# Performance work log

Measured on AMD Instinct MI355X. Metric: run time of the kernel, lower is better.

Reference implementation:

```python
import jax, jax.numpy as jnp
import numpy as np

EMBED = 2048
HEADS = 32
HEAD_DIM = EMBED // HEADS
ALPHA = 12.0
MAX_SEQ = 1024
GAMMA = -ALPHA / MAX_SEQ  # clipped softmax lower stretch
ETA = 1.0


def setup_inputs() -> dict:
    key = jax.random.key(0)
    ks = jax.random.split(key, 12)
    B, T, E, H, D = 4, 1024, EMBED, HEADS, HEAD_DIM
    s = 1.0 / np.sqrt(E)
    hidden_states = jax.random.normal(ks[0], (B, T, E), dtype=jnp.float32)
    # causal attention mask: True = attend
    causal = jnp.tril(jnp.ones((T, T), dtype=bool))
    attention_mask = jnp.broadcast_to(causal[None, None], (B, 1, T, T))
    Wq = jax.random.normal(ks[1], (E, E), dtype=jnp.float32) * s
    bq = jnp.zeros((E,), dtype=jnp.float32)
    Wk = jax.random.normal(ks[2], (E, E), dtype=jnp.float32) * s
    bk = jnp.zeros((E,), dtype=jnp.float32)
    Wv = jax.random.normal(ks[3], (E, E), dtype=jnp.float32) * s
    bv = jnp.zeros((E,), dtype=jnp.float32)
    Wo = jax.random.normal(ks[4], (E, E), dtype=jnp.float32) * s
    bo = jnp.zeros((E,), dtype=jnp.float32)
    gate_w = jax.random.normal(ks[5], (H, D), dtype=jnp.float32) * (1.0 / np.sqrt(D))
    gate_b = jnp.zeros((H,), dtype=jnp.float32)
    return {"hidden_states": hidden_states, "attention_mask": attention_mask,
            "Wq": Wq, "bq": bq, "Wk": Wk, "bk": bk, "Wv": Wv, "bv": bv,
            "Wo": Wo, "bo": bo, "gate_w": gate_w, "gate_b": gate_b}


def clipped_softmax(x, gamma, eta):
    p = jax.nn.softmax(x, axis=-1)
    return jnp.clip((eta - gamma) * p + gamma, 0.0, 1.0)


def reference(hidden_states, attention_mask, Wq, bq, Wk, bk, Wv, bv, Wo, bo, gate_w, gate_b):
    B, T, E = hidden_states.shape
    H, D = HEADS, HEAD_DIM
    scaling = D ** -0.5
    neg_min = jnp.finfo(hidden_states.dtype).min

    q = ((hidden_states @ Wq.T + bq) * scaling).reshape(B, T, H, D)
    k = (hidden_states @ Wk.T + bk).reshape(B, T, H, D)
    v = (hidden_states @ Wv.T + bv).reshape(B, T, H, D)

    # scores: [B,H,T,S]
    scores = jnp.einsum('bthd,bshd->bhts', q, k)
    mask_add = jnp.where(attention_mask, 0.0, neg_min)  # [B,1,T,S]
    scores = jnp.maximum(scores + mask_add, neg_min)

    probs = clipped_softmax(scores, GAMMA, ETA)

    attn_out = jnp.einsum('bhts,bshd->bhtd', probs, v)  # [B,H,T,D]

    # conditional_per_token gate: per-head Linear(head_dim -> 1), sigmoid
    x_heads = hidden_states.reshape(B, T, H, D)
    gate = jax.nn.sigmoid(jnp.einsum('bthd,hd->bht', x_heads, gate_w) + gate_b[None, :, None])
    attn_out = attn_out * gate[..., None]  # gate_scaling_factor = 1.0

    out = attn_out.transpose(0, 2, 1, 3).reshape(B, T, E)
    return out @ Wo.T + bo
```

## Files before the change

kernel.cpp:

```cpp
#include <hip/hip_runtime.h>
#include <hip/hip_bf16.h>

typedef unsigned short ushort_t;
using short8 = __attribute__((ext_vector_type(8))) short;
using f32x4  = __attribute__((ext_vector_type(4))) float;

constexpr int B_ = 4;
constexpr int T_ = 1024;
constexpr int E_ = 2048;
constexpr int H_ = 32;
constexpr int D_ = 64;
constexpr float GAMMA_  = -12.0f / 1024.0f;
constexpr float ONE_MG_ = 1.0f - GAMMA_;

__device__ __forceinline__ ushort_t f2bf(float f) {
  union { float f; unsigned int i; } x; x.f = f;
  unsigned int u = x.i;
  u += 0x7fffu + ((u >> 16) & 1u);
  return (ushort_t)(u >> 16);
}

__global__ __launch_bounds__(256) void f2bf_multi(
    const float* __restrict__ x,
    const float* __restrict__ Wq, const float* __restrict__ Wk,
    const float* __restrict__ Wv, const float* __restrict__ Wo,
    ushort_t* __restrict__ xb,
    ushort_t* __restrict__ wqb, ushort_t* __restrict__ wkb,
    ushort_t* __restrict__ wvb, ushort_t* __restrict__ wob) {
  const int i = blockIdx.x * 256 + threadIdx.x;
  const float* src; ushort_t* dst; int off;
  if (i < 2097152)      { src = x;  dst = xb;  off = i; }
  else if (i < 3145728) { src = Wq; dst = wqb; off = i - 2097152; }
  else if (i < 4194304) { src = Wk; dst = wkb; off = i - 3145728; }
  else if (i < 5242880) { src = Wv; dst = wvb; off = i - 4194304; }
  else                  { src = Wo; dst = wob; off = i - 5242880; }
  const float4 f = ((const float4*)src)[off];
  ushort4 u; u.x = f2bf(f.x); u.y = f2bf(f.y); u.z = f2bf(f.z); u.w = f2bf(f.w);
  ((ushort4*)dst)[off] = u;
}

__device__ __forceinline__ void gl_lds16(const ushort_t* g, ushort_t* l) {
  __builtin_amdgcn_global_load_lds(
      (const __attribute__((address_space(1))) void*)g,
      (__attribute__((address_space(3))) void*)l, 16, 0, 0);
}

__global__ __launch_bounds__(256) void gemm_qkv(
    const ushort_t* __restrict__ xb,
    const ushort_t* __restrict__ wq, const ushort_t* __restrict__ wk,
    const ushort_t* __restrict__ wv,
    const float* __restrict__ bq, const float* __restrict__ bk,
    const float* __restrict__ bv,
    ushort_t* __restrict__ qout, ushort_t* __restrict__ kout,
    ushort_t* __restrict__ vtout) {
  constexpr int K = 2048;
  __shared__ ushort_t As[128 * 32];
  __shared__ ushort_t Bs[128 * 32];
  const int which = blockIdx.x >> 4;
  const int colt  = blockIdx.x & 15;
  const ushort_t* Wt  = (which == 0) ? wq : (which == 1) ? wk : wv;
  const float*   bias = (which == 0) ? bq : (which == 1) ? bk : bv;
  const float    scale = (which == 0) ? 0.125f : 1.0f;

  const int tid = threadIdx.x;
  const int wave = tid >> 6, lane = tid & 63;
  const int lane15 = lane & 15, quad = lane >> 4;
  const int row0 = blockIdx.y * 128, col0 = colt * 128;
  const int srow = lane >> 2;
  const int scol = (lane & 3) * 8;
  const ushort_t* Ag0 = xb + (size_t)(row0 + wave * 32 + srow) * K + scol;
  const ushort_t* Ag1 = Ag0 + 16 * (size_t)K;
  const ushort_t* Bg0 = Wt + (size_t)(col0 + wave * 32 + srow) * K + scol;
  const ushort_t* Bg1 = Bg0 + 16 * (size_t)K;
  ushort_t* Al0 = &As[(wave * 32     ) * 32];
  ushort_t* Al1 = &As[(wave * 32 + 16) * 32];
  ushort_t* Bl0 = &Bs[(wave * 32     ) * 32];
  ushort_t* Bl1 = &Bs[(wave * 32 + 16) * 32];
  const int wr = wave >> 1, wc = wave & 1;
  const int q8 = quad * 8;

  f32x4 acc[4][4];
#pragma unroll
  for (int i = 0; i < 4; i++)
#pragma unroll
    for (int j = 0; j < 4; j++) acc[i][j] = (f32x4){0.f, 0.f, 0.f, 0.f};

  for (int k0 = 0; k0 < K; k0 += 32) {
    __syncthreads();
    gl_lds16(Ag0 + k0, Al0);
    gl_lds16(Ag1 + k0, Al1);
    gl_lds16(Bg0 + k0, Bl0);
    gl_lds16(Bg1 + k0, Bl1);
    __syncthreads();
    short8 a_f[4], b_f[4];
#pragma unroll
    for (int i = 0; i < 4; i++)
      a_f[i] = *(const short8*)&As[(wr * 64 + i * 16 + lane15) * 32 + q8];
#pragma unroll
    for (int j = 0; j < 4; j++)
      b_f[j] = *(const short8*)&Bs[(wc * 64 + j * 16 + lane15) * 32 + q8];
#pragma unroll
    for (int i = 0; i < 4; i++)
#pragma unroll
      for (int j = 0; j < 4; j++)
        acc[i][j] = __builtin_amdgcn_mfma_f32_16x16x32_bf16(
            a_f[i], b_f[j], acc[i][j], 0, 0, 0);
  }

  ushort_t* outp = (which == 0) ? qout : (which == 1) ? kout : vtout;
#pragma unroll
  for (int j = 0; j < 4; j++) {
    const int c = col0 + wc * 64 + j * 16 + lane15;
    const float bia = bias[c];
#pragma unroll
    for (int i = 0; i < 4; i++) {
#pragma unroll
      for (int reg = 0; reg < 4; reg++) {
        const int r = row0 + wr * 64 + i * 16 + quad * 4 + reg;
        const float val = (acc[i][j][reg] + bia) * scale;
        const int b = r >> 10, t = r & 1023, h = c >> 6, d = c & 63;
        if (which < 2)
          outp[(((size_t)(b * 32 + h)) * 1024 + t) * 64 + d] = f2bf(val);
        else
          outp[(((size_t)(b * 32 + h)) * 64 + d) * 1024 + t] = f2bf(val);
      }
    }
  }
}

__global__ __launch_bounds__(256) void gemm_out(
    const ushort_t* __restrict__ A, const ushort_t* __restrict__ Wt,
    const float* __restrict__ bias, float* __restrict__ Cout) {
  constexpr int K = 2048;
  __shared__ ushort_t As[128 * 32];
  __shared__ ushort_t Bs[128 * 32];
  const int tid = threadIdx.x;
  const int wave = tid >> 6, lane = tid & 63;
  const int lane15 = lane & 15, quad = lane >> 4;
  const int row0 = blockIdx.y * 128, col0 = blockIdx.x * 128;
  const int srow = lane >> 2;
  const int scol = (lane & 3) * 8;
  const ushort_t* Ag0 = A  + (size_t)(row0 + wave * 32 + srow) * K + scol;
  const ushort_t* Ag1 = Ag0 + 16 * (size_t)K;
  const ushort_t* Bg0 = Wt + (size_t)(col0 + wave * 32 + srow) * K + scol;
  const ushort_t* Bg1 = Bg0 + 16 * (size_t)K;
  ushort_t* Al0 = &As[(wave * 32     ) * 32];
  ushort_t* Al1 = &As[(wave * 32 + 16) * 32];
  ushort_t* Bl0 = &Bs[(wave * 32     ) * 32];
  ushort_t* Bl1 = &Bs[(wave * 32 + 16) * 32];
  const int wr = wave >> 1, wc = wave & 1;
  const int q8 = quad * 8;

  f32x4 acc[4][4];
#pragma unroll
  for (int i = 0; i < 4; i++)
#pragma unroll
    for (int j = 0; j < 4; j++) acc[i][j] = (f32x4){0.f, 0.f, 0.f, 0.f};

  for (int k0 = 0; k0 < K; k0 += 32) {
    __syncthreads();
    gl_lds16(Ag0 + k0, Al0);
    gl_lds16(Ag1 + k0, Al1);
    gl_lds16(Bg0 + k0, Bl0);
    gl_lds16(Bg1 + k0, Bl1);
    __syncthreads();
    short8 a_f[4], b_f[4];
#pragma unroll
    for (int i = 0; i < 4; i++)
      a_f[i] = *(const short8*)&As[(wr * 64 + i * 16 + lane15) * 32 + q8];
#pragma unroll
    for (int j = 0; j < 4; j++)
      b_f[j] = *(const short8*)&Bs[(wc * 64 + j * 16 + lane15) * 32 + q8];
#pragma unroll
    for (int i = 0; i < 4; i++)
#pragma unroll
      for (int j = 0; j < 4; j++)
        acc[i][j] = __builtin_amdgcn_mfma_f32_16x16x32_bf16(
            a_f[i], b_f[j], acc[i][j], 0, 0, 0);
  }

#pragma unroll
  for (int j = 0; j < 4; j++) {
    const int c = col0 + wc * 64 + j * 16 + lane15;
    const float bia = bias[c];
#pragma unroll
    for (int i = 0; i < 4; i++) {
#pragma unroll
      for (int reg = 0; reg < 4; reg++) {
        const int r = row0 + wr * 64 + i * 16 + quad * 4 + reg;
        Cout[(size_t)r * 2048 + c] = acc[i][j][reg] + bia;
      }
    }
  }
}

__global__ __launch_bounds__(256) void gates_kernel(
    const float* __restrict__ x, const float* __restrict__ gw,
    const float* __restrict__ gb, float* __restrict__ gates) {
  const int idx = blockIdx.x * 256 + threadIdx.x;
  const int h = idx & 31;
  const int bt = idx >> 5;
  const float* xp = x + (size_t)bt * E_ + h * D_;
  const float* wp = gw + h * D_;
  float s = 0.f;
#pragma unroll
  for (int d = 0; d < D_; d += 4) {
    const float4 xv = *(const float4*)&xp[d];
    const float4 wv = *(const float4*)&wp[d];
    s = fmaf(xv.x, wv.x, s); s = fmaf(xv.y, wv.y, s);
    s = fmaf(xv.z, wv.z, s); s = fmaf(xv.w, wv.w, s);
  }
  s += gb[h];
  gates[idx] = 1.0f / (1.0f + __expf(-s));
}

__global__ __launch_bounds__(256) void attn_mfma(
    const ushort_t* __restrict__ q, const ushort_t* __restrict__ k,
    const ushort_t* __restrict__ vt, const float* __restrict__ gates,
    ushort_t* __restrict__ attn_out) {
  __shared__ ushort_t Kt[64 * 72];
  __shared__ ushort_t Vt[64 * 72];
  __shared__ ushort_t Pb[4][16 * 72];

  const int tid = threadIdx.x;
  const int wave = tid >> 6, lane = tid & 63;
  const int l15 = lane & 15, quad = lane >> 4;
  const int bx = blockIdx.x;
  const int qt = 7 - (bx >> 7);
  const int bh = bx & 127;
  const int h = bh & 31, b = bh >> 5;
  const int t0 = qt * 128;
  const int qt8 = qt * 8;
  const ushort_t* qbase = q  + (size_t)bh * (T_ * D_);
  const ushort_t* kbase = k  + (size_t)bh * (T_ * D_);
  const ushort_t* vbase = vt + (size_t)bh * (D_ * T_);

  short8 qf[2][2];
#pragma unroll
  for (int s = 0; s < 2; s++) {
    const ushort_t* qp =
        qbase + (size_t)(t0 + s * 64 + wave * 16 + l15) * 64 + quad * 8;
    qf[s][0] = *(const short8*)qp;
    qf[s][1] = *(const short8*)(qp + 32);
  }

  const int srow = tid >> 2;
  const int scol = (tid & 3) * 16;
  const int nkt = 2 * qt + 2;

  float l_part[2][4] = {};

  for (int kt = 0; kt < nkt; kt++) {
    __syncthreads();
    {
      const ushort_t* kg = &kbase[(size_t)(kt * 64 + srow) * 64 + scol];
      ushort_t* kl = &Kt[srow * 72 + scol];
      *(short8*)kl = *(const short8*)kg;
      *(short8*)(kl + 8) = *(const short8*)(kg + 8);
    }
    __syncthreads();
#pragma unroll
    for (int s = 0; s < 2; s++) {
      const int rb = qt8 + s * 4 + wave;
      if (kt * 4 > rb) continue;
      f32x4 sc[4];
#pragma unroll
      for (int j = 0; j < 4; j++) {
        const int cb = kt * 4 + j;
        if (cb > rb) {
          sc[j] = (f32x4){-3.0e38f, -3.0e38f, -3.0e38f, -3.0e38f};
          continue;
        }
        const ushort_t* kp = &Kt[(j * 16 + l15) * 72 + quad * 8];
        const short8 kf0 = *(const short8*)kp;
        const short8 kf1 = *(const short8*)(kp + 32);
        f32x4 z = (f32x4){0.f, 0.f, 0.f, 0.f};
        z = __builtin_amdgcn_mfma_f32_16x16x32_bf16(qf[s][0], kf0, z, 0, 0, 0);
        z = __builtin_amdgcn_mfma_f32_16x16x32_bf16(qf[s][1], kf1, z, 0, 0, 0);
        if (cb == rb) {
#pragma unroll
          for (int r = 0; r < 4; r++)
            if (l15 > quad * 4 + r) z[r] = -3.0e38f;
        }
        sc[j] = z;
      }
#pragma unroll
      for (int r = 0; r < 4; r++)
        l_part[s][r] += __expf(sc[0][r]) + __expf(sc[1][r]) +
                        __expf(sc[2][r]) + __expf(sc[3][r]);
    }
  }

  float c1[2][4];
#pragma unroll
  for (int s = 0; s < 2; s++)
#pragma unroll
    for (int r = 0; r < 4; r++) {
      float e = l_part[s][r];
      e += __shfl_xor(e, 1); e += __shfl_xor(e, 2);
      e += __shfl_xor(e, 4); e += __shfl_xor(e, 8);
      c1[s][r] = ONE_MG_ / e;
    }

  f32x4 acc[2][4];
#pragma unroll
  for (int s = 0; s < 2; s++)
#pragma unroll
    for (int jd = 0; jd < 4; jd++) acc[s][jd] = (f32x4){0.f, 0.f, 0.f, 0.f};

  for (int kt = 0; kt < nkt; kt++) {
    __syncthreads();
    {
      const ushort_t* kg = &kbase[(size_t)(kt * 64 + srow) * 64 + scol];
      ushort_t* kl = &Kt[srow * 72 + scol];
      *(short8*)kl = *(const short8*)kg;
      *(short8*)(kl + 8) = *(const short8*)(kg + 8);
      const ushort_t* vg = &vbase[(size_t)srow * 1024 + kt * 64 + scol];
      ushort_t* vl = &Vt[srow * 72 + scol];
      *(short8*)vl = *(const short8*)vg;
      *(short8*)(vl + 8) = *(const short8*)(vg + 8);
    }
    __syncthreads();
#pragma unroll
    for (int s = 0; s < 2; s++) {
      const int rb = qt8 + s * 4 + wave;
      if (kt * 4 > rb) continue;
      f32x4 sc[4];
#pragma unroll
      for (int j = 0; j < 4; j++) {
        const int cb = kt * 4 + j;
        if (cb > rb) {
          sc[j] = (f32x4){-3.0e38f, -3.0e38f, -3.0e38f, -3.0e38f};
          continue;
        }
        const ushort_t* kp = &Kt[(j * 16 + l15) * 72 + quad * 8];
        const short8 kf0 = *(const short8*)kp;
        const short8 kf1 = *(const short8*)(kp + 32);
        f32x4 z = (f32x4){0.f, 0.f, 0.f, 0.f};
        z = __builtin_amdgcn_mfma_f32_16x16x32_bf16(qf[s][0], kf0, z, 0, 0, 0);
        z = __builtin_amdgcn_mfma_f32_16x16x32_bf16(qf[s][1], kf1, z, 0, 0, 0);
        if (cb == rb) {
#pragma unroll
          for (int r = 0; r < 4; r++)
            if (l15 > quad * 4 + r) z[r] = -3.0e38f;
        }
        sc[j] = z;
      }
      ushort_t* pb = &Pb[wave][0];
#pragma unroll
      for (int j = 0; j < 4; j++) {
#pragma unroll
        for (int r = 0; r < 4; r++) {
          float p = fmaf(c1[s][r], __expf(sc[j][r]), GAMMA_);
          p = fminf(fmaxf(p, 0.f), 1.f);
          pb[(quad * 4 + r) * 72 + j * 16 + l15] = f2bf(p);
        }
      }
      const short8 pf0 = *(const short8*)&pb[l15 * 72 + quad * 8];
      const short8 pf1 = *(const short8*)&pb[l15 * 72 + 32 + quad * 8];
#pragma unroll
      for (int jd = 0; jd < 4; jd++) {
        const ushort_t* vp = &Vt[(jd * 16 + l15) * 72 + quad * 8];
        const short8 vf0 = *(const short8*)vp;
        const short8 vf1 = *(const short8*)(vp + 32);
        acc[s][jd] =
            __builtin_amdgcn_mfma_f32_16x16x32_bf16(pf0, vf0, acc[s][jd], 0, 0, 0);
        acc[s][jd] =
            __builtin_amdgcn_mfma_f32_16x16x32_bf16(pf1, vf1, acc[s][jd], 0, 0, 0);
      }
    }
  }

#pragma unroll
  for (int s = 0; s < 2; s++) {
#pragma unroll
    for (int r = 0; r < 4; r++) {
      const int t = t0 + s * 64 + wave * 16 + quad * 4 + r;
      const float g = gates[((size_t)b * T_ + t) * H_ + h];
      ushort_t* op = attn_out + ((size_t)b * T_ + t) * E_ + h * 64;
#pragma unroll
      for (int jd = 0; jd < 4; jd++)
        op[jd * 16 + l15] = f2bf(acc[s][jd][r] * g);
    }
  }
}

extern "C" void kernel_launch(void* const* d_in, const int* in_sizes, int n_in,
                              void* d_out, int out_size, void* d_ws, size_t ws_size,
                              hipStream_t stream) {
  (void)in_sizes; (void)n_in; (void)out_size; (void)ws_size;
  const float* x  = (const float*)d_in[0];
  const float* Wq = (const float*)d_in[2];
  const float* bq = (const float*)d_in[3];
  const float* Wk = (const float*)d_in[4];
  const float* bk = (const float*)d_in[5];
  const float* Wv = (const float*)d_in[6];
  const float* bv = (const float*)d_in[7];
  const float* Wo = (const float*)d_in[8];
  const float* bo = (const float*)d_in[9];
  const float* gw = (const float*)d_in[10];
  const float* gb = (const float*)d_in[11];
  float* out = (float*)d_out;

  char* W = (char*)d_ws;
  ushort_t* xb  = (ushort_t*)(W + 0);
  ushort_t* wqb = (ushort_t*)(W + 16777216);
  ushort_t* wkb = (ushort_t*)(W + 25165824);
  ushort_t* wvb = (ushort_t*)(W + 33554432);
  ushort_t* wob = (ushort_t*)(W + 41943040);
  ushort_t* qb  = (ushort_t*)(W + 50331648);
  ushort_t* kb  = (ushort_t*)(W + 67108864);
  ushort_t* vtb = (ushort_t*)(W + 83886080);
  ushort_t* ab  = (ushort_t*)(W + 100663296);
  float*    gts = (float*)(W + 117440512);

  f2bf_multi<<<24576, 256, 0, stream>>>(x, Wq, Wk, Wv, Wo,
                                        xb, wqb, wkb, wvb, wob);

  gemm_qkv<<<dim3(48, 32), 256, 0, stream>>>(xb, wqb, wkb, wvb,
                                             bq, bk, bv, qb, kb, vtb);
  gates_kernel<<<512, 256, 0, stream>>>(x, gw, gb, gts);
  attn_mfma<<<1024, 256, 0, stream>>>(qb, kb, vtb, gts, ab);
  gemm_out<<<dim3(16, 32), 256, 0, stream>>>(ab, wob, bo, out);
}
```

Baseline: 426.6 us.

## Fold log2e into Q scale, sync-free first pass, truncating bf16 probs

Multiplies the Q projection scale by log2(e) so the softmax can use exp2f in place of __expf. The first denominator pass now reads K fragments straight from global memory with no LDS staging or barriers, and reuses each K fragment for both query sub-tiles. Probabilities are cast to bf16 by truncation instead of round-to-nearest, which is cheaper but adds a small downward bias. The risks are more global/L2 traffic in the first pass and a slight loss of accuracy.

```diff
diff --git a/kernel.cpp b/kernel.cpp
--- a/kernel.cpp
+++ b/kernel.cpp
@@ -12,12 +12,17 @@
 constexpr int D_ = 64;
 constexpr float GAMMA_  = -12.0f / 1024.0f;
 constexpr float ONE_MG_ = 1.0f - GAMMA_;
+constexpr float LOG2E_  = 1.44269504088896f;
 
 __device__ __forceinline__ ushort_t f2bf(float f) {
   union { float f; unsigned int i; } x; x.f = f;
   unsigned int u = x.i;
   u += 0x7fffu + ((u >> 16) & 1u);
   return (ushort_t)(u >> 16);
+}
+__device__ __forceinline__ ushort_t f2bf_trunc(float f) {
+  union { float f; unsigned int i; } x; x.f = f;
+  return (ushort_t)(x.i >> 16);
 }
 
 __global__ __launch_bounds__(256) void f2bf_multi(
@@ -60,7 +65,7 @@
   const int colt  = blockIdx.x & 15;
   const ushort_t* Wt  = (which == 0) ? wq : (which == 1) ? wk : wv;
   const float*   bias = (which == 0) ? bq : (which == 1) ? bk : bv;
-  const float    scale = (which == 0) ? 0.125f : 1.0f;
+  const float    scale = (which == 0) ? 0.125f * LOG2E_ : 1.0f;
 
   const int tid = threadIdx.x;
   const int wave = tid >> 6, lane = tid & 63;
@@ -247,8 +252,53 @@
   const int srow = tid >> 2;
   const int scol = (tid & 3) * 16;
   const int nkt = 2 * qt + 2;
+  const int rb1 = qt8 + 4 + wave;
 
   float l_part[2][4] = {};
+
+  for (int kt = 0; kt < nkt; kt++) {
+#pragma unroll
+    for (int j = 0; j < 4; j++) {
+      const int cb = kt * 4 + j;
+      if (cb > rb1) continue;
+      const ushort_t* kp =
+          kbase + (size_t)(kt * 64 + j * 16 + l15) * 64 + quad * 8;
+      const short8 kf0 = *(const short8*)kp;
+      const short8 kf1 = *(const short8*)(kp + 32);
+#pragma unroll
+      for (int s = 0; s < 2; s++) {
+        const int rb = qt8 + s * 4 + wave;
+        if (cb > rb) continue;
+        f32x4 z = (f32x4){0.f, 0.f, 0.f, 0.f};
+        z = __builtin_amdgcn_mfma_f32_16x16x32_bf16(qf[s][0], kf0, z, 0, 0, 0);
+        z = __builtin_amdgcn_mfma_f32_16x16x32_bf16(qf[s][1], kf1, z, 0, 0, 0);
+        if (cb == rb) {
+#pragma unroll
+          for (int r = 0; r < 4; r++)
+            if (l15 > quad * 4 + r) z[r] = -3.0e38f;
+        }
+#pragma unroll
+        for (int r = 0; r < 4; r++) l_part[s][r] += exp2f(z[r]);
+      }
+    }
+  }
+
+  float c1[2][4];
+#pragma unroll
+  for (int s = 0; s < 2; s++)
+#pragma unroll
+    for (int r = 0; r < 4; r++) {
+      float e = l_part[s][r];
+      e += __shfl_xor(e, 1); e += __shfl_xor(e, 2);
+      e += __shfl_xor(e, 4); e += __shfl_xor(e, 8);
+      c1[s][r] = ONE_MG_ / e;
+    }
+
+  f32x4 acc[2][4];
+#pragma unroll
+  for (int s = 0; s < 2; s++)
+#pragma unroll
+    for (int jd = 0; jd < 4; jd++) acc[s][jd] = (f32x4){0.f, 0.f, 0.f, 0.f};
 
   for (int kt = 0; kt < nkt; kt++) {
     __syncthreads();
@@ -257,6 +307,10 @@
       ushort_t* kl = &Kt[srow * 72 + scol];
       *(short8*)kl = *(const short8*)kg;
       *(short8*)(kl + 8) = *(const short8*)(kg + 8);
+      const ushort_t* vg = &vbase[(size_t)srow * 1024 + kt * 64 + scol];
+      ushort_t* vl = &Vt[srow * 72 + scol];
+      *(short8*)vl = *(const short8*)vg;
+      *(short8*)(vl + 8) = *(const short8*)(vg + 8);
     }
     __syncthreads();
 #pragma unroll
@@ -284,76 +338,14 @@
         }
         sc[j] = z;
       }
-#pragma unroll
-      for (int r = 0; r < 4; r++)
-        l_part[s][r] += __expf(sc[0][r]) + __expf(sc[1][r]) +
-                        __expf(sc[2][r]) + __expf(sc[3][r]);
-    }
-  }
-
-  float c1[2][4];
-#pragma unroll
-  for (int s = 0; s < 2; s++)
-#pragma unroll
-    for (int r = 0; r < 4; r++) {
-      float e = l_part[s][r];
-      e += __shfl_xor(e, 1); e += __shfl_xor(e, 2);
-      e += __shfl_xor(e, 4); e += __shfl_xor(e, 8);
-      c1[s][r] = ONE_MG_ / e;
-    }
-
-  f32x4 acc[2][4];
-#pragma unroll
-  for (int s = 0; s < 2; s++)
-#pragma unroll
-    for (int jd = 0; jd < 4; jd++) acc[s][jd] = (f32x4){0.f, 0.f, 0.f, 0.f};
-
-  for (int kt = 0; kt < nkt; kt++) {
-    __syncthreads();
-    {
-      const ushort_t* kg = &kbase[(size_t)(kt * 64 + srow) * 64 + scol];
-      ushort_t* kl = &Kt[srow * 72 + scol];
-      *(short8*)kl = *(const short8*)kg;
-      *(short8*)(kl + 8) = *(const short8*)(kg + 8);
-      const ushort_t* vg = &vbase[(size_t)srow * 1024 + kt * 64 + scol];
-      ushort_t* vl = &Vt[srow * 72 + scol];
-      *(short8*)vl = *(const short8*)vg;
-      *(short8*)(vl + 8) = *(const short8*)(vg + 8);
-    }
-    __syncthreads();
-#pragma unroll
-    for (int s = 0; s < 2; s++) {
-      const int rb = qt8 + s * 4 + wave;
-      if (kt * 4 > rb) continue;
-      f32x4 sc[4];
+      ushort_t* pb = &Pb[wave][0];
 #pragma unroll
       for (int j = 0; j < 4; j++) {
-        const int cb = kt * 4 + j;
-        if (cb > rb) {
-          sc[j] = (f32x4){-3.0e38f, -3.0e38f, -3.0e38f, -3.0e38f};
-          continue;
-        }
-        const ushort_t* kp = &Kt[(j * 16 + l15) * 72 + quad * 8];
-        const short8 kf0 = *(const short8*)kp;
-        const short8 kf1 = *(const short8*)(kp + 32);
-        f32x4 z = (f32x4){0.f, 0.f, 0.f, 0.f};
-        z = __builtin_amdgcn_mfma_f32_16x16x32_bf16(qf[s][0], kf0, z, 0, 0, 0);
-        z = __builtin_amdgcn_mfma_f32_16x16x32_bf16(qf[s][1], kf1, z, 0, 0, 0);
-        if (cb == rb) {
-#pragma unroll
-          for (int r = 0; r < 4; r++)
-            if (l15 > quad * 4 + r) z[r] = -3.0e38f;
-        }
-        sc[j] = z;
-      }
-      ushort_t* pb = &Pb[wave][0];
-#pragma unroll
-      for (int j = 0; j < 4; j++) {
 #pragma unroll
         for (int r = 0; r < 4; r++) {
-          float p = fmaf(c1[s][r], __expf(sc[j][r]), GAMMA_);
+          float p = fmaf(c1[s][r], exp2f(sc[j][r]), GAMMA_);
           p = fminf(fmaxf(p, 0.f), 1.f);
-          pb[(quad * 4 + r) * 72 + j * 16 + l15] = f2bf(p);
+          pb[(quad * 4 + r) * 72 + j * 16 + l15] = f2bf_trunc(p);
         }
       }
       const short8 pf0 = *(const short8*)&pb[l15 * 72 + quad * 8];
```

Result: slower. 442.5 us (+3.7%).
